# Optimization experiments

Hardware: AMD Instinct MI355X
Metric: run time of the kernel (lower is better)

## Reference

```python
import jax, jax.numpy as jnp
import numpy as np

BLOCK_SIZE = 32
EPS = 1e-6


def setup_inputs() -> dict:
    key = jax.random.key(0)
    k1, k2, k3, k4, k5 = jax.random.split(key, 5)
    B, H, L, D = 2, 16, 4096, 128
    return {
        "query_states": jax.random.normal(k1, (B, H, L, D), dtype=jnp.float32),
        "key_states": jax.random.normal(k2, (B, H, L, D), dtype=jnp.float32),
        "value_states": jax.random.normal(k3, (B, H, L, D), dtype=jnp.float32),
        # learned params; init near torch defaults (ones/zeros) with small noise
        "phi_scale": 1.0 + 0.1 * jax.random.normal(k4, (H, 1, D), dtype=jnp.float32),
        "phi_bias": 0.1 * jax.random.normal(k5, (H, 1, D), dtype=jnp.float32),
    }


def _forward(query_states, key_states, value_states, phi_scale, phi_bias):
    B, H, L, D = query_states.shape
    bs = BLOCK_SIZE
    N = L // bs  # L chosen divisible by block_size (no padding path)

    def feature_map(x):  # x: (B,H,N,bs,D)
        # phi_scale (H,1,D) -> (H,1,1,D) broadcasts over (B,H,N,bs,D)
        y = jax.nn.elu(x * phi_scale[:, None] + phi_bias[:, None]) + 1.0
        return jnp.clip(y, 0.0, 10.0)

    q = query_states.reshape(B, H, N, bs, D)
    k = key_states.reshape(B, H, N, bs, D)
    v = value_states.reshape(B, H, N, bs, D)

    phi_q = feature_map(q)
    phi_k = feature_map(k)

    # move block axis to front for scan: (N,B,H,bs,D)
    pq = jnp.moveaxis(phi_q, 2, 0)
    pk = jnp.moveaxis(phi_k, 2, 0)
    vb = jnp.moveaxis(v, 2, 0)

    S0 = jnp.zeros((B, H, D, D), dtype=jnp.float32)
    Z0 = jnp.zeros((B, H, D), dtype=jnp.float32)

    def step(carry, inp):
        S, Z = carry
        pq_n, pk_n, v_n = inp  # each (B,H,bs,D)
        # block-causal, bidirectional within block: update state BEFORE output
        S = S + jnp.einsum('bhkd,bhke->bhde', pk_n, v_n)
        Z = Z + pk_n.sum(axis=-2)
        num = jnp.einsum('bhqd,bhde->bhqe', pq_n, S)
        den = jnp.maximum(jnp.einsum('bhqd,bhd->bhq', pq_n, Z), EPS)
        return (S, Z), num / den[..., None]

    _, out_blocks = jax.lax.scan(step, (S0, Z0), (pq, pk, vb))  # (N,B,H,bs,D)
    out = jnp.moveaxis(out_blocks, 0, 2).reshape(B, H, L, D)
    return out


def reference(query_states, key_states, value_states, phi_scale, phi_bias):
    return _forward(query_states, key_states, value_states, phi_scale, phi_bias)
```

## Files before the change

kernel.cpp:

```cpp
#include <hip/hip_runtime.h>
#include <stdint.h>

#define BH 32
#define LSEQ 4096
#define DDIM 128
#define CHUNKS 16
#define CHUNK_ROWS 256
#define STATE_SZ (DDIM*DDIM + DDIM)

typedef __attribute__((ext_vector_type(8))) short bf16x8;
typedef __attribute__((ext_vector_type(4))) float f32x4;

__device__ inline uint16_t f2bf(float f) {
    uint32_t x = __builtin_bit_cast(uint32_t, f);
    x += 0x7fffu + ((x >> 16) & 1u);
    return (uint16_t)(x >> 16);
}
__device__ inline uint32_t pack2(float a, float b) {
    return (uint32_t)f2bf(a) | ((uint32_t)f2bf(b) << 16);
}
__device__ inline float phi_f(float x, float s, float b) {
    float y = fmaf(x, s, b);
    float pos = fminf(y + 1.0f, 10.0f);
    float neg = __expf(y);
    return (y > 0.0f) ? pos : neg;
}
__device__ inline void bar_lgkm() {
    asm volatile("s_waitcnt lgkmcnt(0)\n\ts_barrier" ::: "memory");
}

#define SMEM1 67584
__global__ __launch_bounds__(512, 2) void la_state(
    const float* __restrict__ K, const float* __restrict__ V,
    const float* __restrict__ scale, const float* __restrict__ bias,
    float* __restrict__ states)
{
    extern __shared__ char smem[];
    const int tid  = threadIdx.x;
    const int bh   = blockIdx.x >> 4;
    const int ch   = blockIdx.x & 15;
    const int h    = bh & 15;
    const int lane = tid & 63;
    const int wid  = tid >> 6;
    const int i15  = lane & 15;
    const int q4   = lane >> 4;
    const size_t base = (size_t)bh * LSEQ * DDIM;
    const int row0 = ch * CHUNK_ROWS;

    const int d  = tid & 127;
    const int rg = tid >> 7;
    const float sk = scale[h*DDIM + d];
    const float bk = bias [h*DDIM + d];

    f32x4 accS[8];
    #pragma unroll
    for (int mt = 0; mt < 8; ++mt) accS[mt] = (f32x4){0.f,0.f,0.f,0.f};
    float zacc = 0.f;

    float kreg[16], vreg[16];
    auto load_kv = [&](int g) {
        const float* Kc = K + base + (size_t)(row0 + 64*g + 16*rg)*DDIM + d;
        const float* Vc = V + base + (size_t)(row0 + 64*g + 16*rg)*DDIM + d;
        #pragma unroll
        for (int j = 0; j < 16; ++j) {
            kreg[j] = Kc[(size_t)j*DDIM];
            vreg[j] = Vc[(size_t)j*DDIM];
        }
    };
    auto stage = [&](int b) {
        uint32_t wk[8], wv8[8];
        #pragma unroll
        for (int j = 0; j < 8; ++j) {
            float p0 = phi_f(kreg[2*j],   sk, bk);
            float p1 = phi_f(kreg[2*j+1], sk, bk);
            zacc += p0 + p1;
            wk[j]  = pack2(p0, p1);
            wv8[j] = pack2(vreg[2*j], vreg[2*j+1]);
        }
        char* pkb = smem + b*16384;
        char* vtb = smem + 32768 + b*16384;
        const uint32_t lin = (uint32_t)(d*128 + 32*rg);
        const uint32_t swz = (uint32_t)((d & 7) << 4);
        *(uint4*)(pkb + ((lin     ) ^ swz)) = ((const uint4*)wk)[0];
        *(uint4*)(pkb + ((lin + 16) ^ swz)) = ((const uint4*)wk)[1];
        *(uint4*)(vtb + ((lin     ) ^ swz)) = ((const uint4*)wv8)[0];
        *(uint4*)(vtb + ((lin + 16) ^ swz)) = ((const uint4*)wv8)[1];
    };

    load_kv(0);
    stage(0);
    load_kv(1);
    bar_lgkm();

    #pragma unroll
    for (int g = 0; g < 4; ++g) {
        if (g < 3) stage((g+1)&1);
        if (g < 2) load_kv(g+2);
        const char* pkb = smem + (g&1)*16384;
        const char* vtb = smem + 32768 + (g&1)*16384;
        const uint32_t swz = (uint32_t)((i15 & 7) << 4);
        #pragma unroll
        for (int ksl = 0; ksl < 2; ++ksl) {
            bf16x8 bv = *(const bf16x8*)(vtb + (((uint32_t)((16*wid+i15)*128 + 64*ksl + 16*q4)) ^ swz));
            #pragma unroll
            for (int mt = 0; mt < 8; ++mt) {
                bf16x8 av = *(const bf16x8*)(pkb + (((uint32_t)((16*mt+i15)*128 + 64*ksl + 16*q4)) ^ swz));
                accS[mt] = __builtin_amdgcn_mfma_f32_16x16x32_bf16(av, bv, accS[mt], 0, 0, 0);
            }
        }
        bar_lgkm();
    }

    float* Zpart = (float*)(smem + 65536);
    Zpart[rg*128 + d] = zacc;
    float* stb = states + (size_t)(bh*CHUNKS + ch)*STATE_SZ;
    #pragma unroll
    for (int mt = 0; mt < 8; ++mt)
        #pragma unroll
        for (int r = 0; r < 4; ++r)
            stb[(size_t)(16*mt + 4*q4 + r)*DDIM + 16*wid + i15] = accS[mt][r];
    bar_lgkm();
    if (tid < 128)
        stb[DDIM*DDIM + tid] = Zpart[tid] + Zpart[128+tid] + Zpart[256+tid] + Zpart[384+tid];
}

__global__ void la_prefix(float* __restrict__ states) {
    const int bh  = blockIdx.y;
    const int idx = blockIdx.x * 128 + threadIdx.x;
    float* p = states + (size_t)bh * CHUNKS * STATE_SZ + idx;
    float run = 0.f;
    #pragma unroll
    for (int c = 0; c < CHUNKS; ++c) {
        float v = p[(size_t)c * STATE_SZ];
        p[(size_t)c * STATE_SZ] = run;
        run += v;
    }
}

#define SMEM2 71168
__global__ __launch_bounds__(512, 2) void la_fwd(
    const float* __restrict__ Q, const float* __restrict__ K,
    const float* __restrict__ V, const float* __restrict__ scale,
    const float* __restrict__ bias, const float* __restrict__ states,
    float* __restrict__ out)
{
    extern __shared__ char smem[];
    char* S0T  = smem;
    char* pkB  = smem + 32768;
    char* vtB  = smem + 49152;
    float* sbL  = (float*)(smem + 69632);
    float* denl = (float*)(smem + 70656);

    const int tid  = threadIdx.x;
    const int b    = blockIdx.x;
    const int lid  = ((b & 7) << 7) | (b >> 3);
    const int half = lid & 1;
    const int cgid = lid >> 1;
    const int bh   = cgid >> 4;
    const int ch   = cgid & 15;
    const int h    = bh & 15;
    const int lane = tid & 63;
    const int wid  = tid >> 6;
    const int i15  = lane & 15;
    const int q4   = lane >> 4;
    const size_t base = (size_t)bh * LSEQ * DDIM;
    const int row0  = ch * CHUNK_ROWS;
    const int qrow0 = row0 + half*128;
    const int NG    = 4 + 4*half;
    const int jm    = 4*half + (wid >> 1);
    const float* stb = states + (size_t)(bh*CHUNKS + ch)*STATE_SZ;

    const int krow = tid >> 4;
    const int kc8  = (tid & 15) * 8;
    const int ve   = tid & 127;
    const int vrg  = tid >> 7;

    float4 kq[2];
    float  vr[8];
    auto load_kv = [&](int g) {
        const float* Kr = K + base + (size_t)(row0 + 32*g + krow)*DDIM + kc8;
        kq[0] = *(const float4*)(Kr);
        kq[1] = *(const float4*)(Kr + 4);
        const float* Vc = V + base + (size_t)(row0 + 32*g + 8*vrg)*DDIM + ve;
        #pragma unroll
        for (int j = 0; j < 8; ++j) vr[j] = Vc[(size_t)j*DDIM];
    };
    auto stage_kv = [&](int bb) {
        float4 s0 = *(const float4*)&sbL[kc8];
        float4 s1 = *(const float4*)&sbL[kc8 + 4];
        float4 b0 = *(const float4*)&sbL[128 + kc8];
        float4 b1 = *(const float4*)&sbL[128 + kc8 + 4];
        uint32_t wk[4];
        wk[0] = pack2(phi_f(kq[0].x, s0.x, b0.x), phi_f(kq[0].y, s0.y, b0.y));
        wk[1] = pack2(phi_f(kq[0].z, s0.z, b0.z), phi_f(kq[0].w, s0.w, b0.w));
        wk[2] = pack2(phi_f(kq[1].x, s1.x, b1.x), phi_f(kq[1].y, s1.y, b1.y));
        wk[3] = pack2(phi_f(kq[1].z, s1.z, b1.z), phi_f(kq[1].w, s1.w, b1.w));
        const uint32_t lin = (uint32_t)(krow*256 + kc8*2);
        const uint32_t swz = (uint32_t)((krow & 7) << 4);
        *(uint4*)(pkB + bb*8192 + (lin ^ swz)) = *(const uint4*)wk;
        uint32_t wv8[4];
        #pragma unroll
        for (int j = 0; j < 4; ++j) wv8[j] = pack2(vr[2*j], vr[2*j+1]);
        *(uint4*)(vtB + bb*10240 + (uint32_t)(ve*80 + vrg*16)) = *(const uint4*)wv8;
    };

    load_kv(0);

    if (tid < 256) sbL[tid] = (tid < 128) ? scale[h*DDIM + tid] : bias[h*DDIM + tid - 128];

    {
        const int se  = tid & 127;
        const int sdg = tid >> 7;
        const uint32_t swz = (uint32_t)((se & 7) << 4);
        #pragma unroll
        for (int pass = 0; pass < 2; ++pass) {
            float sv[16];
            const float* sp = stb + (size_t)(32*sdg + 16*pass)*DDIM + se;
            #pragma unroll
            for (int k2 = 0; k2 < 16; ++k2) sv[k2] = sp[(size_t)k2*DDIM];
            uint32_t wbuf[8];
            #pragma unroll
            for (int k2 = 0; k2 < 8; ++k2) wbuf[k2] = pack2(sv[2*k2], sv[2*k2+1]);
            const uint32_t linb = (uint32_t)(se*256 + (32*sdg + 16*pass)*2);
            *(uint4*)(S0T + ((linb     ) ^ swz)) = ((const uint4*)wbuf)[0];
            *(uint4*)(S0T + ((linb + 16) ^ swz)) = ((const uint4*)wbuf)[1];
        }
    }

    bf16x8 pq[4];
    float dden = 0.f;
    #pragma unroll
    for (int ks = 0; ks < 4; ++ks) {
        const float* sp = scale + h*DDIM + 32*ks + 8*q4;
        const float* bp = bias  + h*DDIM + 32*ks + 8*q4;
        const float* zp = stb + DDIM*DDIM + 32*ks + 8*q4;
        float4 s0 = *(const float4*)sp, s1 = *(const float4*)(sp+4);
        float4 b0 = *(const float4*)bp, b1 = *(const float4*)(bp+4);
        float4 z0 = *(const float4*)zp, z1 = *(const float4*)(zp+4);
        const float* qp = Q + base + (size_t)(qrow0 + 16*wid + i15)*DDIM + 32*ks + 8*q4;
        float4 a0 = *(const float4*)qp, a1 = *(const float4*)(qp+4);
        float f0 = phi_f(a0.x, s0.x, b0.x), f1 = phi_f(a0.y, s0.y, b0.y);
        float f2 = phi_f(a0.z, s0.z, b0.z), f3 = phi_f(a0.w, s0.w, b0.w);
        float f4 = phi_f(a1.x, s1.x, b1.x), f5 = phi_f(a1.y, s1.y, b1.y);
        float f6 = phi_f(a1.z, s1.z, b1.z), f7 = phi_f(a1.w, s1.w, b1.w);
        dden += f0*z0.x + f1*z0.y + f2*z0.z + f3*z0.w
              + f4*z1.x + f5*z1.y + f6*z1.z + f7*z1.w;
        uint4 uu = { pack2(f0,f1), pack2(f2,f3), pack2(f4,f5), pack2(f6,f7) };
        pq[ks] = __builtin_bit_cast(bf16x8, uu);
    }

    stage_kv(0);
    load_kv(1);
    bar_lgkm();

    f32x4 acc[8];
    #pragma unroll
    for (int et = 0; et < 8; ++et) acc[et] = (f32x4){0.f,0.f,0.f,0.f};
    {
        const uint32_t swz = (uint32_t)((i15 & 7) << 4);
        #pragma unroll
        for (int ks = 0; ks < 4; ++ks)
            #pragma unroll
            for (int et = 0; et < 8; ++et) {
                bf16x8 sb = *(const bf16x8*)(S0T + (((uint32_t)((16*et+i15)*256 + (32*ks + 8*q4)*2)) ^ swz));
                acc[et] = __builtin_amdgcn_mfma_f32_16x16x32_bf16(pq[ks], sb, acc[et], 0, 0, 0);
            }
    }
    stage_kv(1);
    if (NG > 2) load_kv(2);
    bar_lgkm();

    char* Ascr = S0T + wid*1280;
    const uint32_t swzf = (uint32_t)((i15 & 7) << 4);

    for (int t = 0; t < NG; ++t) {
        if (t >= 1) {
            if (t + 1 < NG) stage_kv((t+1)&1);
            if (t + 2 < NG) load_kv(t+2);
        }
        const char* pk = pkB + (t&1)*8192;
        const char* vt = vtB + (t&1)*10240;
        if (t <= jm) {
            f32x4 Aacc[2];
            Aacc[0] = (f32x4){0.f,0.f,0.f,0.f};
            Aacc[1] = (f32x4){0.f,0.f,0.f,0.f};
            #pragma unroll
            for (int ks = 0; ks < 4; ++ks) {
                bf16x8 ak0 = *(const bf16x8*)(pk + (((uint32_t)((     i15)*256 + (32*ks + 8*q4)*2)) ^ swzf));
                bf16x8 ak1 = *(const bf16x8*)(pk + (((uint32_t)((16 + i15)*256 + (32*ks + 8*q4)*2)) ^ swzf));
                Aacc[0] = __builtin_amdgcn_mfma_f32_16x16x32_bf16(ak0, pq[ks], Aacc[0], 0, 0, 0);
                Aacc[1] = __builtin_amdgcn_mfma_f32_16x16x32_bf16(ak1, pq[ks], Aacc[1], 0, 0, 0);
            }
            dden += Aacc[0][0]+Aacc[0][1]+Aacc[0][2]+Aacc[0][3]
                  + Aacc[1][0]+Aacc[1][1]+Aacc[1][2]+Aacc[1][3];
            #pragma unroll
            for (int sub = 0; sub < 2; ++sub) {
                uint2 o;
                o.x = pack2(Aacc[sub][0], Aacc[sub][1]);
                o.y = pack2(Aacc[sub][2], Aacc[sub][3]);
                *(uint2*)(Ascr + (uint32_t)((i15*40 + 16*sub + 4*q4)*2)) = o;
            }
            bf16x8 aq = *(const bf16x8*)(Ascr + (uint32_t)((i15*40 + 8*q4)*2));
            #pragma unroll
            for (int et = 0; et < 8; ++et) {
                bf16x8 bv = *(const bf16x8*)(vt + (uint32_t)((16*et+i15)*80 + q4*16));
                acc[et] = __builtin_amdgcn_mfma_f32_16x16x32_bf16(aq, bv, acc[et], 0, 0, 0);
            }
        }
        bar_lgkm();
    }

    dden += __shfl_xor(dden, 16, 64);
    dden += __shfl_xor(dden, 32, 64);
    if (q4 == 0) denl[wid*16 + i15] = dden;
    float inv[4];
    #pragma unroll
    for (int r = 0; r < 4; ++r)
        inv[r] = 1.0f / fmaxf(denl[wid*16 + 4*q4 + r], 1e-6f);
    #pragma unroll
    for (int et = 0; et < 8; ++et)
        #pragma unroll
        for (int r = 0; r < 4; ++r)
            out[base + (size_t)(qrow0 + 16*wid + 4*q4 + r)*DDIM + 16*et + i15] =
                acc[et][r] * inv[r];
}

extern "C" void kernel_launch(void* const* d_in, const int* in_sizes, int n_in,
                              void* d_out, int out_size, void* d_ws, size_t ws_size,
                              hipStream_t stream) {
    const float* Q     = (const float*)d_in[0];
    const float* K     = (const float*)d_in[1];
    const float* V     = (const float*)d_in[2];
    const float* scale = (const float*)d_in[3];
    const float* bias  = (const float*)d_in[4];
    float* out    = (float*)d_out;
    float* states = (float*)d_ws;

    static bool s_attr = false;
    if (!s_attr) {
        hipFuncSetAttribute(reinterpret_cast<const void*>(la_state),
                            hipFuncAttributeMaxDynamicSharedMemorySize, SMEM1);
        hipFuncSetAttribute(reinterpret_cast<const void*>(la_fwd),
                            hipFuncAttributeMaxDynamicSharedMemorySize, SMEM2);
        s_attr = true;
    }

    hipLaunchKernelGGL(la_state, dim3(BH*CHUNKS), dim3(512), SMEM1, stream,
                       K, V, scale, bias, states);
    hipLaunchKernelGGL(la_prefix, dim3(129, BH), dim3(128), 0, stream, states);
    hipLaunchKernelGGL(la_fwd, dim3(BH*CHUNKS*2), dim3(512), SMEM2, stream,
                       Q, K, V, scale, bias, states, out);
}
```

Before: 290.9 us.

## Shrink la_state staging tiles, vectorize prefix scan, raise occupancy bounds

```diff
diff --git a/kernel.cpp b/kernel.cpp
--- a/kernel.cpp
+++ b/kernel.cpp
@@ -29,8 +29,8 @@
     asm volatile("s_waitcnt lgkmcnt(0)\n\ts_barrier" ::: "memory");
 }
 
-#define SMEM1 67584
-__global__ __launch_bounds__(512, 2) void la_state(
+#define SMEM1 34816
+__global__ __launch_bounds__(512, 4) void la_state(
     const float* __restrict__ K, const float* __restrict__ V,
     const float* __restrict__ scale, const float* __restrict__ bias,
     float* __restrict__ states)
@@ -57,34 +57,29 @@
     for (int mt = 0; mt < 8; ++mt) accS[mt] = (f32x4){0.f,0.f,0.f,0.f};
     float zacc = 0.f;
 
-    float kreg[16], vreg[16];
+    float kreg[8], vreg[8];
     auto load_kv = [&](int g) {
-        const float* Kc = K + base + (size_t)(row0 + 64*g + 16*rg)*DDIM + d;
-        const float* Vc = V + base + (size_t)(row0 + 64*g + 16*rg)*DDIM + d;
-        #pragma unroll
-        for (int j = 0; j < 16; ++j) {
+        const float* Kc = K + base + (size_t)(row0 + 32*g + 8*rg)*DDIM + d;
+        const float* Vc = V + base + (size_t)(row0 + 32*g + 8*rg)*DDIM + d;
+        #pragma unroll
+        for (int j = 0; j < 8; ++j) {
             kreg[j] = Kc[(size_t)j*DDIM];
             vreg[j] = Vc[(size_t)j*DDIM];
         }
     };
     auto stage = [&](int b) {
-        uint32_t wk[8], wv8[8];
-        #pragma unroll
-        for (int j = 0; j < 8; ++j) {
+        uint32_t wk[4], wv[4];
+        #pragma unroll
+        for (int j = 0; j < 4; ++j) {
             float p0 = phi_f(kreg[2*j],   sk, bk);
             float p1 = phi_f(kreg[2*j+1], sk, bk);
             zacc += p0 + p1;
-            wk[j]  = pack2(p0, p1);
-            wv8[j] = pack2(vreg[2*j], vreg[2*j+1]);
-        }
-        char* pkb = smem + b*16384;
-        char* vtb = smem + 32768 + b*16384;
-        const uint32_t lin = (uint32_t)(d*128 + 32*rg);
-        const uint32_t swz = (uint32_t)((d & 7) << 4);
-        *(uint4*)(pkb + ((lin     ) ^ swz)) = ((const uint4*)wk)[0];
-        *(uint4*)(pkb + ((lin + 16) ^ swz)) = ((const uint4*)wk)[1];
-        *(uint4*)(vtb + ((lin     ) ^ swz)) = ((const uint4*)wv8)[0];
-        *(uint4*)(vtb + ((lin + 16) ^ swz)) = ((const uint4*)wv8)[1];
+            wk[j] = pack2(p0, p1);
+            wv[j] = pack2(vreg[2*j], vreg[2*j+1]);
+        }
+        const uint32_t off = ((uint32_t)(d*64 + rg*16)) ^ ((uint32_t)((d&7)<<4));
+        *(uint4*)(smem + b*8192 + off)         = *(const uint4*)wk;
+        *(uint4*)(smem + 16384 + b*8192 + off) = *(const uint4*)wv;
     };
 
     load_kv(0);
@@ -92,26 +87,22 @@
     load_kv(1);
     bar_lgkm();
 
-    #pragma unroll
-    for (int g = 0; g < 4; ++g) {
-        if (g < 3) stage((g+1)&1);
-        if (g < 2) load_kv(g+2);
-        const char* pkb = smem + (g&1)*16384;
-        const char* vtb = smem + 32768 + (g&1)*16384;
-        const uint32_t swz = (uint32_t)((i15 & 7) << 4);
-        #pragma unroll
-        for (int ksl = 0; ksl < 2; ++ksl) {
-            bf16x8 bv = *(const bf16x8*)(vtb + (((uint32_t)((16*wid+i15)*128 + 64*ksl + 16*q4)) ^ swz));
-            #pragma unroll
-            for (int mt = 0; mt < 8; ++mt) {
-                bf16x8 av = *(const bf16x8*)(pkb + (((uint32_t)((16*mt+i15)*128 + 64*ksl + 16*q4)) ^ swz));
-                accS[mt] = __builtin_amdgcn_mfma_f32_16x16x32_bf16(av, bv, accS[mt], 0, 0, 0);
-            }
+    for (int g = 0; g < 8; ++g) {
+        if (g + 1 < 8) stage((g+1)&1);
+        if (g + 2 < 8) load_kv(g+2);
+        const char* pkb = smem + (g&1)*8192;
+        const char* vtb = smem + 16384 + (g&1)*8192;
+        const uint32_t swz = (uint32_t)((i15&7)<<4);
+        bf16x8 bv = *(const bf16x8*)(vtb + (((uint32_t)((16*wid+i15)*64 + q4*16)) ^ swz));
+        #pragma unroll
+        for (int mt = 0; mt < 8; ++mt) {
+            bf16x8 av = *(const bf16x8*)(pkb + (((uint32_t)((16*mt+i15)*64 + q4*16)) ^ swz));
+            accS[mt] = __builtin_amdgcn_mfma_f32_16x16x32_bf16(av, bv, accS[mt], 0, 0, 0);
         }
         bar_lgkm();
     }
 
-    float* Zpart = (float*)(smem + 65536);
+    float* Zpart = (float*)(smem + 32768);
     Zpart[rg*128 + d] = zacc;
     float* stb = states + (size_t)(bh*CHUNKS + ch)*STATE_SZ;
     #pragma unroll
@@ -127,18 +118,19 @@
 __global__ void la_prefix(float* __restrict__ states) {
     const int bh  = blockIdx.y;
     const int idx = blockIdx.x * 128 + threadIdx.x;
-    float* p = states + (size_t)bh * CHUNKS * STATE_SZ + idx;
-    float run = 0.f;
+    if (idx >= STATE_SZ/4) return;
+    float4* p = (float4*)(states + (size_t)bh * CHUNKS * STATE_SZ) + idx;
+    float4 run = {0.f, 0.f, 0.f, 0.f};
     #pragma unroll
     for (int c = 0; c < CHUNKS; ++c) {
-        float v = p[(size_t)c * STATE_SZ];
-        p[(size_t)c * STATE_SZ] = run;
-        run += v;
+        float4 v = p[(size_t)c * (STATE_SZ/4)];
+        p[(size_t)c * (STATE_SZ/4)] = run;
+        run.x += v.x; run.y += v.y; run.z += v.z; run.w += v.w;
     }
 }
 
 #define SMEM2 71168
-__global__ __launch_bounds__(512, 2) void la_fwd(
+__global__ __launch_bounds__(512, 4) void la_fwd(
     const float* __restrict__ Q, const float* __restrict__ K,
     const float* __restrict__ V, const float* __restrict__ scale,
     const float* __restrict__ bias, const float* __restrict__ states,
@@ -174,6 +166,8 @@
     const int kc8  = (tid & 15) * 8;
     const int ve   = tid & 127;
     const int vrg  = tid >> 7;
+    const int se  = tid & 127;
+    const int sdg = tid >> 7;
 
     float4 kq[2];
     float  vr[8];
@@ -198,32 +192,28 @@
         const uint32_t lin = (uint32_t)(krow*256 + kc8*2);
         const uint32_t swz = (uint32_t)((krow & 7) << 4);
         *(uint4*)(pkB + bb*8192 + (lin ^ swz)) = *(const uint4*)wk;
-        uint32_t wv8[4];
-        #pragma unroll
-        for (int j = 0; j < 4; ++j) wv8[j] = pack2(vr[2*j], vr[2*j+1]);
-        *(uint4*)(vtB + bb*10240 + (uint32_t)(ve*80 + vrg*16)) = *(const uint4*)wv8;
+        uint32_t wv[4];
+        #pragma unroll
+        for (int j = 0; j < 4; ++j) wv[j] = pack2(vr[2*j], vr[2*j+1]);
+        *(uint4*)(vtB + bb*10240 + (uint32_t)(ve*80 + vrg*16)) = *(const uint4*)wv;
     };
 
     load_kv(0);
-
     if (tid < 256) sbL[tid] = (tid < 128) ? scale[h*DDIM + tid] : bias[h*DDIM + tid - 128];
 
     {
-        const int se  = tid & 127;
-        const int sdg = tid >> 7;
         const uint32_t swz = (uint32_t)((se & 7) << 4);
         #pragma unroll
-        for (int pass = 0; pass < 2; ++pass) {
-            float sv[16];
-            const float* sp = stb + (size_t)(32*sdg + 16*pass)*DDIM + se;
-            #pragma unroll
-            for (int k2 = 0; k2 < 16; ++k2) sv[k2] = sp[(size_t)k2*DDIM];
-            uint32_t wbuf[8];
-            #pragma unroll
-            for (int k2 = 0; k2 < 8; ++k2) wbuf[k2] = pack2(sv[2*k2], sv[2*k2+1]);
-            const uint32_t linb = (uint32_t)(se*256 + (32*sdg + 16*pass)*2);
-            *(uint4*)(S0T + ((linb     ) ^ swz)) = ((const uint4*)wbuf)[0];
-            *(uint4*)(S0T + ((linb + 16) ^ swz)) = ((const uint4*)wbuf)[1];
+        for (int p = 0; p < 4; ++p) {
+            const int d0 = 32*sdg + 8*p;
+            float sv[8];
+            const float* sp = stb + (size_t)d0*DDIM + se;
+            #pragma unroll
+            for (int j = 0; j < 8; ++j) sv[j] = sp[(size_t)j*DDIM];
+            uint32_t w[4];
+            #pragma unroll
+            for (int j = 0; j < 4; ++j) w[j] = pack2(sv[2*j], sv[2*j+1]);
+            *(uint4*)(S0T + (((uint32_t)(se*256 + d0*2)) ^ swz)) = *(const uint4*)w;
         }
     }
 
@@ -249,9 +239,9 @@
         pq[ks] = __builtin_bit_cast(bf16x8, uu);
     }
 
+    bar_lgkm();
     stage_kv(0);
     load_kv(1);
-    bar_lgkm();
 
     f32x4 acc[8];
     #pragma unroll
@@ -267,7 +257,7 @@
             }
     }
     stage_kv(1);
-    if (NG > 2) load_kv(2);
+    load_kv(2);
     bar_lgkm();
 
     char* Ascr = S0T + wid*1280;
@@ -338,8 +328,6 @@
 
     static bool s_attr = false;
     if (!s_attr) {
-        hipFuncSetAttribute(reinterpret_cast<const void*>(la_state),
-                            hipFuncAttributeMaxDynamicSharedMemorySize, SMEM1);
         hipFuncSetAttribute(reinterpret_cast<const void*>(la_fwd),
                             hipFuncAttributeMaxDynamicSharedMemorySize, SMEM2);
         s_attr = true;
@@ -347,7 +335,7 @@
 
     hipLaunchKernelGGL(la_state, dim3(BH*CHUNKS), dim3(512), SMEM1, stream,
                        K, V, scale, bias, states);
-    hipLaunchKernelGGL(la_prefix, dim3(129, BH), dim3(128), 0, stream, states);
+    hipLaunchKernelGGL(la_prefix, dim3(33, BH), dim3(128), 0, stream, states);
     hipLaunchKernelGGL(la_fwd, dim3(BH*CHUNKS*2), dim3(512), SMEM2, stream,
                        Q, K, V, scale, bias, states, out);
 }
```

Result: faster. 277.0 us (-4.8%).
